# Kernel tuning notes

Measured on AMD Instinct MI355X. Metric: run time of the kernel, lower is better.

## Reference

```python
import jax, jax.numpy as jnp
import numpy as np

FEAT_STRIDE = 16
RPN_NEG, RPN_POS = 0.3, 0.7
FG_FRAC, RPN_BATCH = 0.5, 256
BATCH, NGT, FH, FW = 32, 20, 64, 100
A = 9


def generate_anchors(base_size=16, ratios=(0.5, 1.0, 2.0), scales=(8, 16, 32)):
    base = np.array([0, 0, base_size - 1, base_size - 1], dtype=np.float64)
    w = base[2] - base[0] + 1
    h = base[3] - base[1] + 1
    cx = base[0] + 0.5 * (w - 1)
    cy = base[1] + 0.5 * (h - 1)
    size = w * h
    anchors = []
    for r in ratios:
        ws = np.round(np.sqrt(size / r))
        hs = np.round(ws * r)
        for s in scales:
            W, H = ws * s, hs * s
            anchors.append([cx - 0.5 * (W - 1), cy - 0.5 * (H - 1),
                            cx + 0.5 * (W - 1), cy + 0.5 * (H - 1)])
    return np.array(anchors, dtype=np.float32)


def bbox_overlaps_batch(anchors, gt_boxes):
    # anchors (T,4), gt_boxes (B,K,5) -> (B,T,K)
    gt = gt_boxes[:, :, :4]
    gw = gt[:, :, 2] - gt[:, :, 0] + 1.0
    gh = gt[:, :, 3] - gt[:, :, 1] + 1.0
    gt_area = (gw * gh)[:, None, :]                      # (B,1,K)
    aw = anchors[:, 2] - anchors[:, 0] + 1.0
    ah = anchors[:, 3] - anchors[:, 1] + 1.0
    a_area = (aw * ah)[None, :, None]                    # (1,T,1)
    gt_zero = ((gw == 1.0) & (gh == 1.0))[:, None, :]
    a_zero = ((aw == 1.0) & (ah == 1.0))[None, :, None]
    iw = jnp.minimum(anchors[None, :, None, 2], gt[:, None, :, 2]) - \
         jnp.maximum(anchors[None, :, None, 0], gt[:, None, :, 0]) + 1.0
    ih = jnp.minimum(anchors[None, :, None, 3], gt[:, None, :, 3]) - \
         jnp.maximum(anchors[None, :, None, 1], gt[:, None, :, 1]) + 1.0
    inter = jnp.maximum(iw, 0.0) * jnp.maximum(ih, 0.0)
    ua = a_area + gt_area - inter
    ov = inter / ua
    ov = jnp.where(gt_zero, 0.0, ov)
    ov = jnp.where(a_zero, -1.0, ov)
    return ov


def bbox_transform_batch(ex_rois, gt_rois):
    # ex_rois (T,4), gt_rois (B,T,4) -> (B,T,4)
    ew = ex_rois[:, 2] - ex_rois[:, 0] + 1.0
    eh = ex_rois[:, 3] - ex_rois[:, 1] + 1.0
    ecx = ex_rois[:, 0] + 0.5 * ew
    ecy = ex_rois[:, 1] + 0.5 * eh
    gw = gt_rois[:, :, 2] - gt_rois[:, :, 0] + 1.0
    gh = gt_rois[:, :, 3] - gt_rois[:, :, 1] + 1.0
    gcx = gt_rois[:, :, 0] + 0.5 * gw
    gcy = gt_rois[:, :, 1] + 0.5 * gh
    dx = (gcx - ecx[None, :]) / ew[None, :]
    dy = (gcy - ecy[None, :]) / eh[None, :]
    dw = jnp.log(gw / ew[None, :])
    dh = jnp.log(gh / eh[None, :])
    return jnp.stack([dx, dy, dw, dh], axis=2)


def _rank_per_row(pri):
    # rank of each element within its row after ascending sort
    return jnp.argsort(jnp.argsort(pri, axis=1), axis=1)


def setup_inputs() -> dict:
    key = jax.random.key(0)
    k1, k2, k3 = jax.random.split(key, 3)
    rpn_cls_score = jax.random.normal(k1, (BATCH, 2 * A, FH, FW), dtype=jnp.float32)
    img_h, img_w = float(FH * FEAT_STRIDE), float(FW * FEAT_STRIDE)
    x1 = jax.random.uniform(k2, (BATCH, NGT)) * (img_w * 0.6)
    y1 = jax.random.uniform(k3, (BATCH, NGT)) * (img_h * 0.6)
    bw = 16.0 + jax.random.uniform(jax.random.fold_in(key, 1), (BATCH, NGT)) * 300.0
    bh = 16.0 + jax.random.uniform(jax.random.fold_in(key, 2), (BATCH, NGT)) * 300.0
    x2 = jnp.minimum(x1 + bw, img_w - 1.0)
    y2 = jnp.minimum(y1 + bh, img_h - 1.0)
    cls = jnp.ones((BATCH, NGT))
    gt = jnp.stack([x1, y1, x2, y2, cls], axis=2)
    valid = (jnp.arange(NGT) < 15).astype(jnp.float32)  # last 5 rows: zero padding
    gt = (gt * valid[None, :, None]).astype(jnp.float32)
    im_info = jnp.tile(jnp.array([[img_h, img_w, 1.0]], dtype=jnp.float32), (BATCH, 1))
    num_boxes = jnp.full((BATCH,), 15, dtype=jnp.int32)
    return {"rpn_cls_score": rpn_cls_score, "gt_boxes": gt,
            "im_info": im_info, "num_boxes": num_boxes}


def reference(rpn_cls_score, gt_boxes, im_info, num_boxes):
    B = gt_boxes.shape[0]
    H, W = rpn_cls_score.shape[2], rpn_cls_score.shape[3]
    anchors0 = jnp.asarray(generate_anchors())           # (A,4)
    sx = jnp.arange(W, dtype=jnp.float32) * FEAT_STRIDE
    sy = jnp.arange(H, dtype=jnp.float32) * FEAT_STRIDE
    SX, SY = jnp.meshgrid(sx, sy)                        # 'xy' indexing, (H,W)
    shifts = jnp.stack([SX.ravel(), SY.ravel(), SX.ravel(), SY.ravel()], axis=1)
    all_anchors = (anchors0[None, :, :] + shifts[:, None, :]).reshape(-1, 4)  # (T,4)
    T = all_anchors.shape[0]

    img_h, img_w = im_info[0, 0], im_info[0, 1]
    inside = (all_anchors[:, 0] >= 0) & (all_anchors[:, 1] >= 0) & \
             (all_anchors[:, 2] < img_w) & (all_anchors[:, 3] < img_h)  # (T,)

    ov = bbox_overlaps_batch(all_anchors, gt_boxes)      # (B,T,K)
    ov_in = jnp.where(inside[None, :, None], ov, -2.0)   # exclude border anchors
    max_ov = jnp.max(ov_in, axis=2)                      # (B,T)
    argmax_ov = jnp.argmax(ov_in, axis=2)                # (B,T)
    gt_max = jnp.max(ov_in, axis=1)                      # (B,K)

    labels = jnp.full((B, T), -1.0, dtype=jnp.float32)
    labels = jnp.where(max_ov < RPN_NEG, 0.0, labels)    # bg (no clobber)
    gt_max = jnp.where(gt_max == 0.0, 1e-5, gt_max)
    keep = jnp.sum((ov_in == gt_max[:, None, :]).astype(jnp.int32), axis=2)
    labels = jnp.where(keep > 0, 1.0, labels)            # best anchor per gt
    labels = jnp.where(max_ov >= RPN_POS, 1.0, labels)   # fg by threshold
    labels = jnp.where(inside[None, :], labels, -1.0)

    # --- random fg/bg subsampling (vectorized random permutation) ---
    key = jax.random.key(42)
    kf, kb = jax.random.split(key)
    num_fg = int(FG_FRAC * RPN_BATCH)
    pri_fg = jnp.where(labels == 1.0, jax.random.uniform(kf, (B, T)), jnp.inf)
    rank_fg = _rank_per_row(pri_fg)
    labels = jnp.where((labels == 1.0) & (rank_fg >= num_fg), -1.0, labels)
    num_bg = RPN_BATCH - jnp.sum((labels == 1.0).astype(jnp.int32), axis=1)  # (B,)
    pri_bg = jnp.where(labels == 0.0, jax.random.uniform(kb, (B, T)), jnp.inf)
    rank_bg = _rank_per_row(pri_bg)
    labels = jnp.where((labels == 0.0) & (rank_bg >= num_bg[:, None]), -1.0, labels)

    gt_assigned = jnp.take_along_axis(gt_boxes, argmax_ov[:, :, None], axis=1)  # (B,T,5)
    bbox_targets = bbox_transform_batch(all_anchors, gt_assigned[:, :, :4])     # (B,T,4)
    bbox_targets = jnp.where(inside[None, :, None], bbox_targets, 0.0)

    bbox_in_w = jnp.where(labels == 1.0, 1.0, 0.0)       # RPN_BBOX_INSIDE_WEIGHTS[0]=1
    num_examples = jnp.sum((labels >= 0.0).astype(jnp.float32), axis=1)         # (B,)
    uw = (1.0 / num_examples)[:, None]
    bbox_out_w = jnp.where((labels == 1.0) | (labels == 0.0), uw, 0.0)

    # --- reshape to dense output layout ---
    labels_o = labels.reshape(B, H, W, A).transpose(0, 3, 1, 2).reshape(B, 1, A * H, W)
    targets_o = bbox_targets.reshape(B, H, W, A * 4).transpose(0, 3, 1, 2)
    in_w_o = jnp.broadcast_to(bbox_in_w[:, :, None], (B, T, 4)) \
        .reshape(B, H, W, 4 * A).transpose(0, 3, 1, 2)
    out_w_o = jnp.broadcast_to(bbox_out_w[:, :, None], (B, T, 4)) \
        .reshape(B, H, W, 4 * A).transpose(0, 3, 1, 2)
    return labels_o, targets_o, in_w_o, out_w_o
```

## Files before the change

### kernel.cpp

```cpp
#include <hip/hip_runtime.h>
#include <stdint.h>

#define JAX_PARTITIONABLE 1

static constexpr int B_   = 32;
static constexpr int NGT_ = 20;
static constexpr int H_   = 64;
static constexpr int W_   = 100;
static constexpr int A_   = 9;
static constexpr int HW_  = H_ * W_;
static constexpr int T_   = HW_ * A_;
static constexpr int NBLK_ = T_ / 256;
static constexpr uint32_t NUMFG_ = 128u;
static constexpr uint32_t RPNBATCH_ = 256u;
static constexpr int OUT0_ = B_ * T_;
static constexpr int OUTC_ = B_ * 4 * A_ * HW_;

struct TF2 { uint32_t a, b; };

__host__ __device__ constexpr uint32_t rotl32(uint32_t v, int r) {
  return (v << r) | (v >> (32 - r));
}

__host__ __device__ constexpr TF2 tf2x32(uint32_t k0, uint32_t k1,
                                         uint32_t x0, uint32_t x1) {
  uint32_t ks2 = k0 ^ k1 ^ 0x1BD11BDAu;
  x0 += k0; x1 += k1;
#define TFR_(r) x0 += x1; x1 = rotl32(x1, (r)); x1 ^= x0;
  TFR_(13) TFR_(15) TFR_(26) TFR_(6)
  x0 += k1;  x1 += ks2 + 1u;
  TFR_(17) TFR_(29) TFR_(16) TFR_(24)
  x0 += ks2; x1 += k0 + 2u;
  TFR_(13) TFR_(15) TFR_(26) TFR_(6)
  x0 += k0;  x1 += k1 + 3u;
  TFR_(17) TFR_(29) TFR_(16) TFR_(24)
  x0 += k1;  x1 += ks2 + 4u;
  TFR_(13) TFR_(15) TFR_(26) TFR_(6)
  x0 += ks2; x1 += k0 + 5u;
#undef TFR_
  return TF2{x0, x1};
}

#if JAX_PARTITIONABLE
static constexpr TF2 KFk = tf2x32(0u, 42u, 0u, 0u);
static constexpr TF2 KBk = tf2x32(0u, 42u, 0u, 1u);
static constexpr uint32_t KF0 = KFk.a, KF1 = KFk.b;
static constexpr uint32_t KB0 = KBk.a, KB1 = KBk.b;
#else
static constexpr TF2 R02 = tf2x32(0u, 42u, 0u, 2u);
static constexpr TF2 R13 = tf2x32(0u, 42u, 1u, 3u);
static constexpr uint32_t KF0 = R02.a, KF1 = R13.a;
static constexpr uint32_t KB0 = R02.b, KB1 = R13.b;
#endif

__device__ inline uint32_t mant23(uint32_t k0, uint32_t k1, uint32_t j) {
#if JAX_PARTITIONABLE
  TF2 r = tf2x32(k0, k1, 0u, j);
  return (r.a ^ r.b) >> 9;
#else
  constexpr uint32_t HALF_ = (uint32_t)((uint64_t)B_ * T_ / 2);
  uint32_t lo = (j < HALF_) ? j : j - HALF_;
  TF2 r = tf2x32(k0, k1, lo, lo + HALF_);
  return ((j < HALF_) ? r.a : r.b) >> 9;
#endif
}

__device__ inline uint32_t fkey(float f) {
  uint32_t u = __float_as_uint(f);
  return (u & 0x80000000u) ? ~u : (u | 0x80000000u);
}

__constant__ float c_anc[9][4] = {
  { -84.f,  -40.f,  99.f,  55.f},
  {-176.f,  -88.f, 191.f, 103.f},
  {-360.f, -184.f, 375.f, 199.f},
  { -56.f,  -56.f,  71.f,  71.f},
  {-120.f, -120.f, 135.f, 135.f},
  {-248.f, -248.f, 263.f, 263.f},
  { -36.f,  -80.f,  51.f,  95.f},
  { -80.f, -168.f,  95.f, 183.f},
  {-168.f, -344.f, 183.f, 359.f},
};

__global__ __launch_bounds__(192) void k1_iou(const float* __restrict__ gt,
                                              const float* __restrict__ im,
                                              uint32_t* __restrict__ gmax,
                                              uint32_t* __restrict__ bkey,
                                              uint32_t* __restrict__ barg) {
#pragma clang fp contract(off)
  const int b = blockIdx.y;
  const int tid = threadIdx.x;
  const int iq = blockIdx.x * 192 + tid;
  __shared__ float4 sbox[NGT_];
  __shared__ float sgar[NGT_];
  __shared__ uint32_t skey[NGT_];
  __shared__ uint32_t smask;

  bool valid = false;
  if (tid < NGT_) {
    const float x1 = gt[(b * NGT_ + tid) * 5 + 0];
    const float y1 = gt[(b * NGT_ + tid) * 5 + 1];
    const float x2 = gt[(b * NGT_ + tid) * 5 + 2];
    const float y2 = gt[(b * NGT_ + tid) * 5 + 3];
    const float gw = x2 - x1 + 1.0f, gh = y2 - y1 + 1.0f;
    valid = !(gw == 1.0f && gh == 1.0f);
    sbox[tid] = make_float4(x1, y1, x2, y2);
    sgar[tid] = gw * gh;
    skey[tid] = 0u;
  }
  unsigned long long mv = __ballot(valid);
  if (tid == 0) smask = (uint32_t)mv;
  __syncthreads();

  const int aa = iq / 1600;
  const int cell0 = (iq % 1600) * 4;
  const float imh = im[0], imw = im[1];
  const float bx1 = c_anc[aa][0], by1 = c_anc[aa][1];
  const float bx2 = c_anc[aa][2], by2 = c_anc[aa][3];

  float ax1[4], ay1[4], ax2[4], ay2[4], aarea[4];
  bool ins[4];
#pragma unroll
  for (int c = 0; c < 4; ++c) {
    const int cell = cell0 + c;
    const int wx = cell % W_, hy = cell / W_;
    ax1[c] = bx1 + wx * 16.0f;
    ay1[c] = by1 + hy * 16.0f;
    ax2[c] = bx2 + wx * 16.0f;
    ay2[c] = by2 + hy * 16.0f;
    ins[c] = (ax1[c] >= 0.0f) && (ay1[c] >= 0.0f) && (ax2[c] < imw) && (ay2[c] < imh);
    aarea[c] = (ax2[c] - ax1[c] + 1.0f) * (ay2[c] - ay1[c] + 1.0f);
  }

  uint32_t bk[4] = {0u, 0u, 0u, 0u};
  uint32_t ba[4] = {0u, 0u, 0u, 0u};
  const uint32_t mask = smask;
  const bool anyin = __ballot(ins[0] || ins[1] || ins[2] || ins[3]) != 0ull;

  if (anyin) {
    for (int g = 0; g < NGT_; ++g) {
      if (!((mask >> g) & 1u)) continue;
      const float4 gb = sbox[g];
      const float gar = sgar[g];
      uint32_t gm = 0u;
#pragma unroll
      for (int c = 0; c < 4; ++c) {
        float iw = fminf(ax2[c], gb.z) - fmaxf(ax1[c], gb.x) + 1.0f;
        float ih = fminf(ay2[c], gb.w) - fmaxf(ay1[c], gb.y) + 1.0f;
        float inter = fmaxf(iw, 0.0f) * fmaxf(ih, 0.0f);
        float ua = aarea[c] + gar - inter;
        float ov = inter / ua;
        uint32_t k = ins[c] ? fkey(ov) : 0u;
        if (k > bk[c]) { bk[c] = k; ba[c] = (uint32_t)g; }
        gm = k > gm ? k : gm;
      }
      for (int d = 1; d < 64; d <<= 1) {
        uint32_t o = (uint32_t)__shfl_xor((int)gm, d, 64);
        gm = (o > gm) ? o : gm;
      }
      if ((tid & 63) == 0) atomicMax(&skey[g], gm);
    }
  }
  __syncthreads();
  if (tid < NGT_) atomicMax(&gmax[b * 32 + tid], skey[tid]);

  const size_t base = (size_t)b * T_ + (size_t)aa * HW_ + cell0;
  *(uint4*)(bkey + base) = make_uint4(bk[0], bk[1], bk[2], bk[3]);
  barg[base >> 2] = ba[0] | (ba[1] << 8) | (ba[2] << 16) | (ba[3] << 24);
}

__global__ __launch_bounds__(256) void k2_label(const float* __restrict__ gt,
                                                const float* __restrict__ im,
                                                const uint32_t* __restrict__ gmax,
                                                const uint32_t* __restrict__ bkey,
                                                int8_t* __restrict__ labels,
                                                uint32_t* __restrict__ cntblk,
                                                uint32_t* __restrict__ cand) {
#pragma clang fp contract(off)
  const int b = blockIdx.y;
  const int bx = blockIdx.x;
  const int tid = threadIdx.x;
  const int i = bx * 256 + tid;
  __shared__ float4 sbox[NGT_];
  __shared__ float sgar[NGT_];
  __shared__ uint32_t skey[NGT_];
  __shared__ uint32_t smask, sminG;
  __shared__ uint32_t sfgc[4], sbgc[4];

  bool valid = false;
  uint32_t myk = 0xFFFFFFFFu;
  if (tid < NGT_) {
    const float x1 = gt[(b * NGT_ + tid) * 5 + 0];
    const float y1 = gt[(b * NGT_ + tid) * 5 + 1];
    const float x2 = gt[(b * NGT_ + tid) * 5 + 2];
    const float y2 = gt[(b * NGT_ + tid) * 5 + 3];
    const float gw = x2 - x1 + 1.0f, gh = y2 - y1 + 1.0f;
    valid = !(gw == 1.0f && gh == 1.0f);
    sbox[tid] = make_float4(x1, y1, x2, y2);
    sgar[tid] = gw * gh;
    const uint32_t gk = gmax[b * 32 + tid];
    skey[tid] = gk;
    if (valid && gk > 0x80000000u) myk = gk;
  }
  unsigned long long mv = __ballot(valid);
  uint32_t mn = myk;
  for (int d = 1; d < 64; d <<= 1) {
    uint32_t o = (uint32_t)__shfl_xor((int)mn, d, 64);
    mn = (o < mn) ? o : mn;
  }
  if (tid == 0) { smask = (uint32_t)mv; sminG = mn; }
  __syncthreads();

  const int a = i / HW_, cell = i % HW_;
  const int t = cell * A_ + a;
  const float imh = im[0], imw = im[1];
  const float ax1 = c_anc[a][0] + (cell % W_) * 16.0f;
  const float ay1 = c_anc[a][1] + (cell / W_) * 16.0f;
  const float ax2 = c_anc[a][2] + (cell % W_) * 16.0f;
  const float ay2 = c_anc[a][3] + (cell / W_) * 16.0f;
  const bool inside = (ax1 >= 0.0f) && (ay1 >= 0.0f) && (ax2 < imw) && (ay2 < imh);
  const float aarea = (ax2 - ax1 + 1.0f) * (ay2 - ay1 + 1.0f);

  const uint32_t bk = bkey[(size_t)b * T_ + i];
  const float maxovf = __uint_as_float(bk & 0x7FFFFFFFu);

  int lab = -1;
  if (inside && maxovf < 0.3f) lab = 0;

  bool haskeep = false;
  const bool needck = inside && bk >= sminG && maxovf < 0.7f;
  if (__ballot(needck) != 0ull) {
    const uint32_t mask = smask;
    for (int g = 0; g < NGT_; ++g) {
      if (!((mask >> g) & 1u)) continue;
      const float4 gb = sbox[g];
      const float gar = sgar[g];
      float iw = fminf(ax2, gb.z) - fmaxf(ax1, gb.x) + 1.0f;
      float ih = fminf(ay2, gb.w) - fmaxf(ay1, gb.y) + 1.0f;
      float inter = fmaxf(iw, 0.0f) * fmaxf(ih, 0.0f);
      float ua = aarea + gar - inter;
      float ov = inter / ua;
      const uint32_t gk = skey[g];
      if (needck && gk > 0x80000000u && fkey(ov) == gk) haskeep = true;
    }
  }
  if (haskeep) lab = 1;
  if (inside && maxovf >= 0.7f) lab = 1;
  labels[(size_t)b * T_ + i] = (int8_t)lab;

  uint32_t m = 0;
  if (lab >= 0)
    m = mant23(lab ? KF0 : KB0, lab ? KF1 : KB1, (uint32_t)(b * T_ + t));

  const int wv = tid >> 6, lane = tid & 63;
  const unsigned long long mk1 = __ballot(lab == 1);
  const unsigned long long mk0 = __ballot(lab == 0);
  if (lane == 0) { sfgc[wv] = (uint32_t)__popcll(mk1); sbgc[wv] = (uint32_t)__popcll(mk0); }
  __syncthreads();
  uint32_t fgbase = 0, bgbase = 0, fgtot = 0, bgtot = 0;
  for (int w2 = 0; w2 < 4; ++w2) {
    if (w2 < wv) { fgbase += sfgc[w2]; bgbase += sbgc[w2]; }
    fgtot += sfgc[w2]; bgtot += sbgc[w2];
  }
  const unsigned long long lmask = (1ull << lane) - 1ull;
  if (lab == 1) {
    uint32_t off = fgbase + (uint32_t)__popcll(mk1 & lmask);
    cand[((size_t)0 * B_ + b) * T_ + (size_t)bx * 256 + off] = m;
  } else if (lab == 0) {
    uint32_t off = bgbase + (uint32_t)__popcll(mk0 & lmask);
    cand[((size_t)1 * B_ + b) * T_ + (size_t)bx * 256 + off] = m;
  }
  if (tid == 0) {
    cntblk[(0 * B_ + b) * NBLK_ + bx] = fgtot;
    cntblk[(1 * B_ + b) * NBLK_ + bx] = bgtot;
  }
}

__device__ inline void find_kth1024(uint32_t* hist, int n, uint32_t target, int tid,
                                    uint32_t* wsum, uint32_t* res) {
  const int C = n >> 10;
  const int base = tid * C;
  uint32_t s = 0;
  for (int i = 0; i < C; ++i) s += hist[base + i];
  uint32_t v = s;
  for (int d = 1; d < 64; d <<= 1) {
    uint32_t u = (uint32_t)__shfl_up((int)v, d, 64);
    if ((tid & 63) >= d) v += u;
  }
  const int wv = tid >> 6;
  if ((tid & 63) == 63) wsum[wv] = v;
  __syncthreads();
  uint32_t woff = 0;
  for (int w2 = 0; w2 < wv; ++w2) woff += wsum[w2];
  uint32_t c = woff + v - s;
  for (int i = 0; i < C; ++i) {
    uint32_t h = hist[base + i];
    if (h != 0u && target >= c && target < c + h) {
      res[0] = (uint32_t)(base + i);
      res[1] = c;
    }
    c += h;
  }
  __syncthreads();
}

__global__ __launch_bounds__(1024) void k3_select(const int8_t* __restrict__ labels,
                                                  const uint32_t* __restrict__ cntblk,
                                                  const uint32_t* __restrict__ cand,
                                                  uint32_t* __restrict__ cnt,
                                                  uint32_t* __restrict__ sel) {
  const int b = blockIdx.x >> 1;
  const int cls = blockIdx.x & 1;
  const int tid = threadIdx.x;
  __shared__ uint32_t scnt[NBLK_];
  __shared__ uint32_t hist[4096];
  __shared__ uint32_t wsum[16];
  __shared__ uint32_t res[2];
  __shared__ uint32_t lcnt, sTot, sCf;

  if (tid == 0) { sTot = 0u; sCf = 0u; }
  __syncthreads();
  if (tid < NBLK_) {
    uint32_t c = cntblk[(cls * B_ + b) * NBLK_ + tid];
    scnt[tid] = c;
    atomicAdd(&sTot, c);
    if (cls == 1) atomicAdd(&sCf, cntblk[(0 * B_ + b) * NBLK_ + tid]);
  }
  __syncthreads();
  const uint32_t n = sTot;
  const uint32_t cf = (cls == 0) ? n : sCf;
  if (tid == 0) cnt[b * 2 + cls] = n;
  const uint32_t fgk = cf < NUMFG_ ? cf : NUMFG_;
  const uint32_t K = (cls == 0) ? NUMFG_ : RPNBATCH_ - fgk;
  if (n <= K) {
    if (tid == 0) { sel[b * 4 + cls * 2] = 0xFFFFFFFFu; sel[b * 4 + cls * 2 + 1] = 0xFFFFFFFFu; }
    return;
  }
  const uint32_t* list = cand + ((size_t)cls * B_ + b) * T_;

  for (int i = tid; i < 2048; i += 1024) hist[i] = 0u;
  __syncthreads();
  for (int gi = tid; gi < T_; gi += 1024)
    if ((uint32_t)(gi & 255) < scnt[gi >> 8]) atomicAdd(&hist[list[gi] >> 12], 1u);
  __syncthreads();
  find_kth1024(hist, 2048, K - 1u, tid, wsum, res);
  const uint32_t b1 = res[0], cb1 = res[1];
  __syncthreads();

  for (int i = tid; i < 4096; i += 1024) hist[i] = 0u;
  __syncthreads();
  for (int gi = tid; gi < T_; gi += 1024)
    if ((uint32_t)(gi & 255) < scnt[gi >> 8]) {
      uint32_t m = list[gi];
      if ((m >> 12) == b1) atomicAdd(&hist[m & 0xFFFu], 1u);
    }
  __syncthreads();
  find_kth1024(hist, 4096, K - 1u - cb1, tid, wsum, res);
  const uint32_t b2 = res[0], cb2 = res[1];
  const uint32_t Mstar = (b1 << 12) | b2;
  const uint32_t need = K - cb1 - cb2;
  const uint32_t cnteq = hist[b2];
  __syncthreads();

  uint32_t tstar = 0xFFFFFFFFu;
  if (need < cnteq) {
    const int8_t want = (cls == 0) ? (int8_t)1 : (int8_t)0;
    const uint32_t k0 = (cls == 0) ? KF0 : KB0;
    const uint32_t k1 = (cls == 0) ? KF1 : KB1;
    const int8_t* lrow = labels + (size_t)b * T_;
    if (tid == 0) lcnt = 0u;
    __syncthreads();
    for (int s = tid; s < T_; s += 1024) {
      if (lrow[s] == want) {
        int aa = s / HW_, cc = s % HW_;
        uint32_t t = (uint32_t)(cc * A_ + aa);
        if (mant23(k0, k1, (uint32_t)b * (uint32_t)T_ + t) == Mstar) {
          uint32_t p = atomicAdd(&lcnt, 1u);
          if (p < 4096u) hist[p] = t;
        }
      }
    }
    __syncthreads();
    if (tid == 0) {
      uint32_t nn = lcnt < 4096u ? lcnt : 4096u;
      uint32_t prev = 0u;
      for (uint32_t kk = 0; kk < need; ++kk) {
        uint32_t mn2 = 0xFFFFFFFFu;
        for (uint32_t i2 = 0; i2 < nn; ++i2) {
          uint32_t vv = hist[i2];
          if ((kk == 0u || vv > prev) && vv < mn2) mn2 = vv;
        }
        prev = mn2;
      }
      tstar = prev;
    }
  }
  if (tid == 0) { sel[b * 4 + cls * 2] = Mstar; sel[b * 4 + cls * 2 + 1] = tstar; }
}

__global__ __launch_bounds__(256) void k4_final(const float* __restrict__ gt,
                                                const float* __restrict__ im,
                                                const int8_t* __restrict__ labels,
                                                const int8_t* __restrict__ argmax8,
                                                const uint32_t* __restrict__ cnt,
                                                const uint32_t* __restrict__ sel,
                                                float* __restrict__ out) {
#pragma clang fp contract(off)
  const int b = blockIdx.y;
  const int tid = threadIdx.x;
  const int i = blockIdx.x * 256 + tid;
  __shared__ float sgt[NGT_ * 5];
  if (tid < NGT_ * 5) sgt[tid] = gt[b * NGT_ * 5 + tid];
  __syncthreads();

  const int a = i / HW_, cell = i % HW_;
  const int t = cell * A_ + a;
  const float imh = im[0], imw = im[1];
  const float ax1 = c_anc[a][0] + (cell % W_) * 16.0f;
  const float ay1 = c_anc[a][1] + (cell / W_) * 16.0f;
  const float ax2 = c_anc[a][2] + (cell % W_) * 16.0f;
  const float ay2 = c_anc[a][3] + (cell / W_) * 16.0f;
  const bool inside = (ax1 >= 0.0f) && (ay1 >= 0.0f) && (ax2 < imw) && (ay2 < imh);

  int lab = labels[(size_t)b * T_ + i];
  const uint32_t j = (uint32_t)(b * T_ + t);
  if (lab == 1) {
    uint32_t m = mant23(KF0, KF1, j);
    uint32_t Ms = sel[b * 4 + 0], ts = sel[b * 4 + 1];
    if (!(m < Ms || (m == Ms && (uint32_t)t <= ts))) lab = -1;
  } else if (lab == 0) {
    uint32_t m = mant23(KB0, KB1, j);
    uint32_t Ms = sel[b * 4 + 2], ts = sel[b * 4 + 3];
    if (!(m < Ms || (m == Ms && (uint32_t)t <= ts))) lab = -1;
  }

  const uint32_t cf = cnt[b * 2 + 0];
  const uint32_t cbn = cnt[b * 2 + 1];
  const uint32_t fgk = cf < NUMFG_ ? cf : NUMFG_;
  const uint32_t nbg = RPNBATCH_ - fgk;
  const uint32_t bgk = cbn < nbg ? cbn : nbg;
  const float uw = 1.0f / (float)(fgk + bgk);

  float tg0 = 0.f, tg1 = 0.f, tg2 = 0.f, tg3 = 0.f;
  if (inside) {
    const int bg_ = argmax8[(size_t)b * T_ + i];
    const float gx1 = sgt[bg_ * 5], gy1 = sgt[bg_ * 5 + 1];
    const float gx2 = sgt[bg_ * 5 + 2], gy2 = sgt[bg_ * 5 + 3];
    const float ew = ax2 - ax1 + 1.0f, eh = ay2 - ay1 + 1.0f;
    const float ecx = ax1 + 0.5f * ew, ecy = ay1 + 0.5f * eh;
    const float gw = gx2 - gx1 + 1.0f, gh = gy2 - gy1 + 1.0f;
    const float gcx = gx1 + 0.5f * gw, gcy = gy1 + 0.5f * gh;
    tg0 = (gcx - ecx) / ew;
    tg1 = (gcy - ecy) / eh;
    tg2 = logf(gw / ew);
    tg3 = logf(gh / eh);
  }
  const float inw = (lab == 1) ? 1.0f : 0.0f;
  const float oww = (lab == 1 || lab == 0) ? uw : 0.0f;

  out[(size_t)b * T_ + i] = (float)lab;
  const size_t ch = ((size_t)b * 36 + (size_t)a * 4) * HW_ + cell;
  float* o1 = out + OUT0_;
  o1[ch] = tg0; o1[ch + HW_] = tg1; o1[ch + 2 * HW_] = tg2; o1[ch + 3 * HW_] = tg3;
  float* o2 = o1 + OUTC_;
  o2[ch] = inw; o2[ch + HW_] = inw; o2[ch + 2 * HW_] = inw; o2[ch + 3 * HW_] = inw;
  float* o3 = o2 + OUTC_;
  o3[ch] = oww; o3[ch + HW_] = oww; o3[ch + 2 * HW_] = oww; o3[ch + 3 * HW_] = oww;
}

extern "C" void kernel_launch(void* const* d_in, const int* in_sizes, int n_in,
                              void* d_out, int out_size, void* d_ws, size_t ws_size,
                              hipStream_t stream) {
  (void)in_sizes; (void)n_in; (void)out_size; (void)ws_size;
  const float* gt = (const float*)d_in[1];
  const float* im = (const float*)d_in[2];
  float* out = (float*)d_out;

  uint8_t* ws = (uint8_t*)d_ws;
  uint32_t* gmax   = (uint32_t*)(ws + 0);
  uint32_t* cnt    = (uint32_t*)(ws + 4096);
  uint32_t* sel    = (uint32_t*)(ws + 4352);
  uint32_t* cntblk = (uint32_t*)(ws + 4864);
  int8_t*   labels = (int8_t*)  (ws + 62464);
  uint32_t* barg   = (uint32_t*)(ws + 1905664);
  uint32_t* bkey   = (uint32_t*)(ws + 3748864);
  uint32_t* cand   = (uint32_t*)(ws + 11121664);

  (void)hipMemsetAsync(ws, 0, 4096, stream);

  k1_iou<<<dim3(75, B_), dim3(192), 0, stream>>>(gt, im, gmax, bkey, barg);
  k2_label<<<dim3(NBLK_, B_), dim3(256), 0, stream>>>(gt, im, gmax, bkey, labels, cntblk, cand);
  k3_select<<<dim3(B_ * 2), dim3(1024), 0, stream>>>(labels, cntblk, cand, cnt, sel);
  k4_final<<<dim3(NBLK_, B_), dim3(256), 0, stream>>>(gt, im, labels, (const int8_t*)barg,
                                                      cnt, sel, out);
}
```

Before: 208.8 us.

## Fuse selection into label kernel via last-block pattern and vectorize per-thread work

Removes the memset and the separate select kernel: k1 writes per-block gt max partials instead of atomics, k2 reduces them itself, and the last block per batch (tracked by an atomic counter) runs the histogram top-k selection. k2 and k4 now process four anchors per thread with vector loads and float4 stores. The cost is that the selection runs on a single 192-thread block per batch rather than 1024-thread blocks, and it adds extra shared memory to every k2 block.

Result: slower. 537.6 us (+157.5%).

```diff
diff --git a/kernel.cpp b/kernel.cpp
--- a/kernel.cpp
+++ b/kernel.cpp
@@ -1,5 +1,6 @@
 #include <hip/hip_runtime.h>
 #include <stdint.h>
+#include <stddef.h>
 
 #define JAX_PARTITIONABLE 1
 
@@ -10,7 +11,8 @@
 static constexpr int A_   = 9;
 static constexpr int HW_  = H_ * W_;
 static constexpr int T_   = HW_ * A_;
-static constexpr int NBLK_ = T_ / 256;
+static constexpr int NB2_ = 75;
+static constexpr int SEG_ = 768;
 static constexpr uint32_t NUMFG_ = 128u;
 static constexpr uint32_t RPNBATCH_ = 256u;
 static constexpr int OUT0_ = B_ * T_;
@@ -84,17 +86,21 @@
 
 __global__ __launch_bounds__(192) void k1_iou(const float* __restrict__ gt,
                                               const float* __restrict__ im,
-                                              uint32_t* __restrict__ gmax,
+                                              uint32_t* __restrict__ gpart,
                                               uint32_t* __restrict__ bkey,
-                                              uint32_t* __restrict__ barg) {
+                                              uint32_t* __restrict__ barg,
+                                              uint32_t* __restrict__ dcnt) {
 #pragma clang fp contract(off)
   const int b = blockIdx.y;
+  const int bx = blockIdx.x;
   const int tid = threadIdx.x;
-  const int iq = blockIdx.x * 192 + tid;
+  const int iq = bx * 192 + tid;
   __shared__ float4 sbox[NGT_];
   __shared__ float sgar[NGT_];
   __shared__ uint32_t skey[NGT_];
   __shared__ uint32_t smask;
+
+  if (bx == 0 && tid == 0) dcnt[b] = 0u;
 
   bool valid = false;
   if (tid < NGT_) {
@@ -162,33 +168,71 @@
     }
   }
   __syncthreads();
-  if (tid < NGT_) atomicMax(&gmax[b * 32 + tid], skey[tid]);
+  if (tid < NGT_) gpart[(b * NGT_ + tid) * NB2_ + bx] = skey[tid];
 
   const size_t base = (size_t)b * T_ + (size_t)aa * HW_ + cell0;
   *(uint4*)(bkey + base) = make_uint4(bk[0], bk[1], bk[2], bk[3]);
   barg[base >> 2] = ba[0] | (ba[1] << 8) | (ba[2] << 16) | (ba[3] << 24);
 }
 
-__global__ __launch_bounds__(256) void k2_label(const float* __restrict__ gt,
+__device__ inline void find_kth128(uint32_t* hist, int n, uint32_t target, int tid,
+                                   uint32_t* wsum, uint32_t* res) {
+  const int C = n >> 7;
+  uint32_t s = 0, v = 0;
+  int base = 0;
+  if (tid < 128) {
+    base = tid * C;
+    for (int i = 0; i < C; ++i) s += hist[base + i];
+    v = s;
+    for (int d = 1; d < 64; d <<= 1) {
+      uint32_t u = (uint32_t)__shfl_up((int)v, d, 64);
+      if ((tid & 63) >= d) v += u;
+    }
+    if ((tid & 63) == 63) wsum[tid >> 6] = v;
+  }
+  __syncthreads();
+  if (tid < 128) {
+    uint32_t woff = (tid >= 64) ? wsum[0] : 0u;
+    uint32_t c = woff + v - s;
+    for (int i = 0; i < C; ++i) {
+      uint32_t h = hist[base + i];
+      if (h != 0u && target >= c && target < c + h) {
+        res[0] = (uint32_t)(base + i);
+        res[1] = c;
+      }
+      c += h;
+    }
+  }
+  __syncthreads();
+}
+
+__global__ __launch_bounds__(192) void k2_label(const float* __restrict__ gt,
                                                 const float* __restrict__ im,
-                                                const uint32_t* __restrict__ gmax,
+                                                const uint32_t* __restrict__ gpart,
                                                 const uint32_t* __restrict__ bkey,
                                                 int8_t* __restrict__ labels,
                                                 uint32_t* __restrict__ cntblk,
-                                                uint32_t* __restrict__ cand) {
+                                                uint32_t* __restrict__ cand,
+                                                uint32_t* __restrict__ dcnt,
+                                                uint32_t* __restrict__ cnt,
+                                                uint32_t* __restrict__ sel) {
 #pragma clang fp contract(off)
   const int b = blockIdx.y;
   const int bx = blockIdx.x;
   const int tid = threadIdx.x;
-  const int i = bx * 256 + tid;
+  const int iq = bx * 192 + tid;
   __shared__ float4 sbox[NGT_];
   __shared__ float sgar[NGT_];
   __shared__ uint32_t skey[NGT_];
-  __shared__ uint32_t smask, sminG;
-  __shared__ uint32_t sfgc[4], sbgc[4];
+  __shared__ uint32_t smask, sminG, sflag;
+  __shared__ uint32_t swc[3];
+  __shared__ uint32_t scnt2[2][NB2_];
+  __shared__ uint32_t hist[4096];
+  __shared__ uint32_t wsum[2];
+  __shared__ uint32_t res[2];
+  __shared__ uint32_t lcnt, stot[2];
 
   bool valid = false;
-  uint32_t myk = 0xFFFFFFFFu;
   if (tid < NGT_) {
     const float x1 = gt[(b * NGT_ + tid) * 5 + 0];
     const float y1 = gt[(b * NGT_ + tid) * 5 + 1];
@@ -198,274 +242,301 @@
     valid = !(gw == 1.0f && gh == 1.0f);
     sbox[tid] = make_float4(x1, y1, x2, y2);
     sgar[tid] = gw * gh;
-    const uint32_t gk = gmax[b * 32 + tid];
-    skey[tid] = gk;
-    if (valid && gk > 0x80000000u) myk = gk;
+    skey[tid] = 0u;
   }
   unsigned long long mv = __ballot(valid);
-  uint32_t mn = myk;
-  for (int d = 1; d < 64; d <<= 1) {
-    uint32_t o = (uint32_t)__shfl_xor((int)mn, d, 64);
-    mn = (o < mn) ? o : mn;
-  }
-  if (tid == 0) { smask = (uint32_t)mv; sminG = mn; }
-  __syncthreads();
-
-  const int a = i / HW_, cell = i % HW_;
-  const int t = cell * A_ + a;
+  if (tid == 0) smask = (uint32_t)mv;
+  __syncthreads();
+  for (int idx = tid; idx < NGT_ * NB2_; idx += 192)
+    atomicMax(&skey[idx / NB2_], gpart[b * NGT_ * NB2_ + idx]);
+  __syncthreads();
+  if (tid < 64) {
+    uint32_t kk = 0xFFFFFFFFu;
+    if (tid < NGT_ && ((smask >> tid) & 1u)) {
+      uint32_t g = skey[tid];
+      if (g > 0x80000000u) kk = g;
+    }
+    for (int d = 1; d < 64; d <<= 1) {
+      uint32_t o = (uint32_t)__shfl_xor((int)kk, d, 64);
+      kk = (o < kk) ? o : kk;
+    }
+    if (tid == 0) sminG = kk;
+  }
+  __syncthreads();
+
+  const int aa = iq / 1600;
+  const int cell0 = (iq % 1600) * 4;
   const float imh = im[0], imw = im[1];
-  const float ax1 = c_anc[a][0] + (cell % W_) * 16.0f;
-  const float ay1 = c_anc[a][1] + (cell / W_) * 16.0f;
-  const float ax2 = c_anc[a][2] + (cell % W_) * 16.0f;
-  const float ay2 = c_anc[a][3] + (cell / W_) * 16.0f;
-  const bool inside = (ax1 >= 0.0f) && (ay1 >= 0.0f) && (ax2 < imw) && (ay2 < imh);
-  const float aarea = (ax2 - ax1 + 1.0f) * (ay2 - ay1 + 1.0f);
-
-  const uint32_t bk = bkey[(size_t)b * T_ + i];
-  const float maxovf = __uint_as_float(bk & 0x7FFFFFFFu);
-
-  int lab = -1;
-  if (inside && maxovf < 0.3f) lab = 0;
-
-  bool haskeep = false;
-  const bool needck = inside && bk >= sminG && maxovf < 0.7f;
-  if (__ballot(needck) != 0ull) {
+  const float bx1 = c_anc[aa][0], by1 = c_anc[aa][1];
+  const float bx2 = c_anc[aa][2], by2 = c_anc[aa][3];
+  const size_t base = (size_t)b * T_ + (size_t)aa * HW_ + cell0;
+  const uint4 bk4 = *(const uint4*)(bkey + base);
+
+  float ax1[4], ay1[4], ax2[4], ay2[4], aarea[4];
+  bool ins[4], need[4];
+  uint32_t bkv[4] = {bk4.x, bk4.y, bk4.z, bk4.w};
+  int lab[4];
+#pragma unroll
+  for (int c = 0; c < 4; ++c) {
+    const int cell = cell0 + c;
+    const int wx = cell % W_, hy = cell / W_;
+    ax1[c] = bx1 + wx * 16.0f;
+    ay1[c] = by1 + hy * 16.0f;
+    ax2[c] = bx2 + wx * 16.0f;
+    ay2[c] = by2 + hy * 16.0f;
+    ins[c] = (ax1[c] >= 0.0f) && (ay1[c] >= 0.0f) && (ax2[c] < imw) && (ay2[c] < imh);
+    aarea[c] = (ax2[c] - ax1[c] + 1.0f) * (ay2[c] - ay1[c] + 1.0f);
+    const float mo = __uint_as_float(bkv[c] & 0x7FFFFFFFu);
+    lab[c] = -1;
+    if (ins[c] && mo < 0.3f) lab[c] = 0;
+    need[c] = ins[c] && bkv[c] >= sminG && mo < 0.7f;
+    if (ins[c] && mo >= 0.7f) lab[c] = 1;
+  }
+  if (__ballot(need[0] || need[1] || need[2] || need[3]) != 0ull) {
     const uint32_t mask = smask;
     for (int g = 0; g < NGT_; ++g) {
       if (!((mask >> g) & 1u)) continue;
+      const uint32_t gk = skey[g];
+      if (gk <= 0x80000000u) continue;
       const float4 gb = sbox[g];
       const float gar = sgar[g];
-      float iw = fminf(ax2, gb.z) - fmaxf(ax1, gb.x) + 1.0f;
-      float ih = fminf(ay2, gb.w) - fmaxf(ay1, gb.y) + 1.0f;
-      float inter = fmaxf(iw, 0.0f) * fmaxf(ih, 0.0f);
-      float ua = aarea + gar - inter;
-      float ov = inter / ua;
-      const uint32_t gk = skey[g];
-      if (needck && gk > 0x80000000u && fkey(ov) == gk) haskeep = true;
-    }
-  }
-  if (haskeep) lab = 1;
-  if (inside && maxovf >= 0.7f) lab = 1;
-  labels[(size_t)b * T_ + i] = (int8_t)lab;
-
-  uint32_t m = 0;
-  if (lab >= 0)
-    m = mant23(lab ? KF0 : KB0, lab ? KF1 : KB1, (uint32_t)(b * T_ + t));
-
-  const int wv = tid >> 6, lane = tid & 63;
-  const unsigned long long mk1 = __ballot(lab == 1);
-  const unsigned long long mk0 = __ballot(lab == 0);
-  if (lane == 0) { sfgc[wv] = (uint32_t)__popcll(mk1); sbgc[wv] = (uint32_t)__popcll(mk0); }
-  __syncthreads();
-  uint32_t fgbase = 0, bgbase = 0, fgtot = 0, bgtot = 0;
-  for (int w2 = 0; w2 < 4; ++w2) {
-    if (w2 < wv) { fgbase += sfgc[w2]; bgbase += sbgc[w2]; }
-    fgtot += sfgc[w2]; bgtot += sbgc[w2];
-  }
-  const unsigned long long lmask = (1ull << lane) - 1ull;
-  if (lab == 1) {
-    uint32_t off = fgbase + (uint32_t)__popcll(mk1 & lmask);
-    cand[((size_t)0 * B_ + b) * T_ + (size_t)bx * 256 + off] = m;
-  } else if (lab == 0) {
-    uint32_t off = bgbase + (uint32_t)__popcll(mk0 & lmask);
-    cand[((size_t)1 * B_ + b) * T_ + (size_t)bx * 256 + off] = m;
+#pragma unroll
+      for (int c = 0; c < 4; ++c) {
+        if (!need[c]) continue;
+        float iw = fminf(ax2[c], gb.z) - fmaxf(ax1[c], gb.x) + 1.0f;
+        float ih = fminf(ay2[c], gb.w) - fmaxf(ay1[c], gb.y) + 1.0f;
+        float inter = fmaxf(iw, 0.0f) * fmaxf(ih, 0.0f);
+        float ua = aarea[c] + gar - inter;
+        float ov = inter / ua;
+        if (fkey(ov) == gk) lab[c] = 1;
+      }
+    }
+  }
+
+  uint32_t lpack = 0, mant[4];
+  int nf = 0, nb = 0;
+#pragma unroll
+  for (int c = 0; c < 4; ++c) {
+    lpack |= ((uint32_t)(uint8_t)(int8_t)lab[c]) << (8 * c);
+    mant[c] = 0u;
+    if (lab[c] >= 0) {
+      const int t = (cell0 + c) * A_ + aa;
+      mant[c] = mant23(lab[c] ? KF0 : KB0, lab[c] ? KF1 : KB1, (uint32_t)(b * T_ + t));
+      if (lab[c] == 1) ++nf; else ++nb;
+    }
+  }
+  *(uint32_t*)(labels + base) = lpack;
+
+  const int lane = tid & 63, wv = tid >> 6;
+  uint32_t cpk = (uint32_t)nf | ((uint32_t)nb << 16);
+  uint32_t incl = cpk;
+  for (int d = 1; d < 64; d <<= 1) {
+    uint32_t u = (uint32_t)__shfl_up((int)incl, d, 64);
+    if (lane >= d) incl += u;
+  }
+  uint32_t wtot = (uint32_t)__shfl((int)incl, 63, 64);
+  if (lane == 0) swc[wv] = wtot;
+  __syncthreads();
+  uint32_t woffF = 0, woffB = 0, totF = 0, totB = 0;
+  for (int w = 0; w < 3; ++w) {
+    uint32_t v = swc[w];
+    if (w < wv) { woffF += v & 0xFFFFu; woffB += v >> 16; }
+    totF += v & 0xFFFFu; totB += v >> 16;
+  }
+  uint32_t excl = incl - cpk;
+  uint32_t posF = woffF + (excl & 0xFFFFu);
+  uint32_t posB = woffB + (excl >> 16);
+  uint32_t* dstF = cand + ((size_t)0 * B_ + b) * T_ + (size_t)bx * SEG_;
+  uint32_t* dstB = cand + ((size_t)1 * B_ + b) * T_ + (size_t)bx * SEG_;
+#pragma unroll
+  for (int c = 0; c < 4; ++c) {
+    if (lab[c] == 1) dstF[posF++] = mant[c];
+    else if (lab[c] == 0) dstB[posB++] = mant[c];
   }
   if (tid == 0) {
-    cntblk[(0 * B_ + b) * NBLK_ + bx] = fgtot;
-    cntblk[(1 * B_ + b) * NBLK_ + bx] = bgtot;
-  }
-}
-
-__device__ inline void find_kth1024(uint32_t* hist, int n, uint32_t target, int tid,
-                                    uint32_t* wsum, uint32_t* res) {
-  const int C = n >> 10;
-  const int base = tid * C;
-  uint32_t s = 0;
-  for (int i = 0; i < C; ++i) s += hist[base + i];
-  uint32_t v = s;
-  for (int d = 1; d < 64; d <<= 1) {
-    uint32_t u = (uint32_t)__shfl_up((int)v, d, 64);
-    if ((tid & 63) >= d) v += u;
-  }
-  const int wv = tid >> 6;
-  if ((tid & 63) == 63) wsum[wv] = v;
-  __syncthreads();
-  uint32_t woff = 0;
-  for (int w2 = 0; w2 < wv; ++w2) woff += wsum[w2];
-  uint32_t c = woff + v - s;
-  for (int i = 0; i < C; ++i) {
-    uint32_t h = hist[base + i];
-    if (h != 0u && target >= c && target < c + h) {
-      res[0] = (uint32_t)(base + i);
-      res[1] = c;
-    }
-    c += h;
-  }
-  __syncthreads();
-}
-
-__global__ __launch_bounds__(1024) void k3_select(const int8_t* __restrict__ labels,
-                                                  const uint32_t* __restrict__ cntblk,
-                                                  const uint32_t* __restrict__ cand,
-                                                  uint32_t* __restrict__ cnt,
-                                                  uint32_t* __restrict__ sel) {
-  const int b = blockIdx.x >> 1;
-  const int cls = blockIdx.x & 1;
-  const int tid = threadIdx.x;
-  __shared__ uint32_t scnt[NBLK_];
-  __shared__ uint32_t hist[4096];
-  __shared__ uint32_t wsum[16];
-  __shared__ uint32_t res[2];
-  __shared__ uint32_t lcnt, sTot, sCf;
-
-  if (tid == 0) { sTot = 0u; sCf = 0u; }
-  __syncthreads();
-  if (tid < NBLK_) {
-    uint32_t c = cntblk[(cls * B_ + b) * NBLK_ + tid];
-    scnt[tid] = c;
-    atomicAdd(&sTot, c);
-    if (cls == 1) atomicAdd(&sCf, cntblk[(0 * B_ + b) * NBLK_ + tid]);
-  }
-  __syncthreads();
-  const uint32_t n = sTot;
-  const uint32_t cf = (cls == 0) ? n : sCf;
-  if (tid == 0) cnt[b * 2 + cls] = n;
-  const uint32_t fgk = cf < NUMFG_ ? cf : NUMFG_;
-  const uint32_t K = (cls == 0) ? NUMFG_ : RPNBATCH_ - fgk;
-  if (n <= K) {
-    if (tid == 0) { sel[b * 4 + cls * 2] = 0xFFFFFFFFu; sel[b * 4 + cls * 2 + 1] = 0xFFFFFFFFu; }
-    return;
-  }
-  const uint32_t* list = cand + ((size_t)cls * B_ + b) * T_;
-
-  for (int i = tid; i < 2048; i += 1024) hist[i] = 0u;
-  __syncthreads();
-  for (int gi = tid; gi < T_; gi += 1024)
-    if ((uint32_t)(gi & 255) < scnt[gi >> 8]) atomicAdd(&hist[list[gi] >> 12], 1u);
-  __syncthreads();
-  find_kth1024(hist, 2048, K - 1u, tid, wsum, res);
-  const uint32_t b1 = res[0], cb1 = res[1];
-  __syncthreads();
-
-  for (int i = tid; i < 4096; i += 1024) hist[i] = 0u;
-  __syncthreads();
-  for (int gi = tid; gi < T_; gi += 1024)
-    if ((uint32_t)(gi & 255) < scnt[gi >> 8]) {
-      uint32_t m = list[gi];
-      if ((m >> 12) == b1) atomicAdd(&hist[m & 0xFFFu], 1u);
-    }
-  __syncthreads();
-  find_kth1024(hist, 4096, K - 1u - cb1, tid, wsum, res);
-  const uint32_t b2 = res[0], cb2 = res[1];
-  const uint32_t Mstar = (b1 << 12) | b2;
-  const uint32_t need = K - cb1 - cb2;
-  const uint32_t cnteq = hist[b2];
-  __syncthreads();
-
-  uint32_t tstar = 0xFFFFFFFFu;
-  if (need < cnteq) {
-    const int8_t want = (cls == 0) ? (int8_t)1 : (int8_t)0;
-    const uint32_t k0 = (cls == 0) ? KF0 : KB0;
-    const uint32_t k1 = (cls == 0) ? KF1 : KB1;
-    const int8_t* lrow = labels + (size_t)b * T_;
-    if (tid == 0) lcnt = 0u;
+    cntblk[(0 * B_ + b) * NB2_ + bx] = totF;
+    cntblk[(1 * B_ + b) * NB2_ + bx] = totB;
+  }
+
+  __threadfence();
+  __syncthreads();
+  if (tid == 0) sflag = (atomicAdd(&dcnt[b], 1u) == (uint32_t)(NB2_ - 1)) ? 1u : 0u;
+  __syncthreads();
+  if (!sflag) return;
+  __threadfence();
+
+  if (tid == 0) { stot[0] = 0u; stot[1] = 0u; }
+  __syncthreads();
+  for (int idx = tid; idx < 2 * NB2_; idx += 192) {
+    const int cls = idx / NB2_, sx = idx % NB2_;
+    const uint32_t v = cntblk[(cls * B_ + b) * NB2_ + sx];
+    scnt2[cls][sx] = v;
+    atomicAdd(&stot[cls], v);
+  }
+  __syncthreads();
+  const uint32_t cf = stot[0], cbn = stot[1];
+  if (tid == 0) { cnt[b * 2 + 0] = cf; cnt[b * 2 + 1] = cbn; }
+
+  for (int cls = 0; cls < 2; ++cls) {
+    const uint32_t fgk = cf < NUMFG_ ? cf : NUMFG_;
+    const uint32_t K = (cls == 0) ? NUMFG_ : RPNBATCH_ - fgk;
+    const uint32_t n = (cls == 0) ? cf : cbn;
+    if (n <= K) {
+      if (tid == 0) { sel[b * 4 + cls * 2] = 0xFFFFFFFFu; sel[b * 4 + cls * 2 + 1] = 0xFFFFFFFFu; }
+      __syncthreads();
+      continue;
+    }
+    const uint32_t* list = cand + ((size_t)cls * B_ + b) * T_;
+
+    for (int i2 = tid; i2 < 2048; i2 += 192) hist[i2] = 0u;
     __syncthreads();
-    for (int s = tid; s < T_; s += 1024) {
-      if (lrow[s] == want) {
-        int aa = s / HW_, cc = s % HW_;
-        uint32_t t = (uint32_t)(cc * A_ + aa);
-        if (mant23(k0, k1, (uint32_t)b * (uint32_t)T_ + t) == Mstar) {
-          uint32_t p = atomicAdd(&lcnt, 1u);
-          if (p < 4096u) hist[p] = t;
+    for (int gi = tid; gi < T_; gi += 192) {
+      const int seg = gi / SEG_, off = gi - seg * SEG_;
+      if ((uint32_t)off < scnt2[cls][seg]) atomicAdd(&hist[list[gi] >> 12], 1u);
+    }
+    __syncthreads();
+    find_kth128(hist, 2048, K - 1u, tid, wsum, res);
+    const uint32_t b1 = res[0], cb1 = res[1];
+
+    for (int i2 = tid; i2 < 4096; i2 += 192) hist[i2] = 0u;
+    __syncthreads();
+    for (int gi = tid; gi < T_; gi += 192) {
+      const int seg = gi / SEG_, off = gi - seg * SEG_;
+      if ((uint32_t)off < scnt2[cls][seg]) {
+        const uint32_t m = list[gi];
+        if ((m >> 12) == b1) atomicAdd(&hist[m & 0xFFFu], 1u);
+      }
+    }
+    __syncthreads();
+    find_kth128(hist, 4096, K - 1u - cb1, tid, wsum, res);
+    const uint32_t b2 = res[0], cb2 = res[1];
+    const uint32_t Mstar = (b1 << 12) | b2;
+    const uint32_t need2 = K - cb1 - cb2;
+    const uint32_t cnteq = hist[b2];
+    __syncthreads();
+
+    uint32_t tstar = 0xFFFFFFFFu;
+    if (need2 < cnteq) {
+      const int8_t want = (cls == 0) ? (int8_t)1 : (int8_t)0;
+      const uint32_t k0 = (cls == 0) ? KF0 : KB0;
+      const uint32_t k1 = (cls == 0) ? KF1 : KB1;
+      const int8_t* lrow = labels + (size_t)b * T_;
+      if (tid == 0) lcnt = 0u;
+      __syncthreads();
+      for (int s = tid; s < T_; s += 192) {
+        if (lrow[s] == want) {
+          const int aa2 = s / HW_, cc = s % HW_;
+          const uint32_t t = (uint32_t)(cc * A_ + aa2);
+          if (mant23(k0, k1, (uint32_t)b * (uint32_t)T_ + t) == Mstar) {
+            const uint32_t p = atomicAdd(&lcnt, 1u);
+            if (p < 4096u) hist[p] = t;
+          }
         }
       }
-    }
+      __syncthreads();
+      if (tid == 0) {
+        const uint32_t nn = lcnt < 4096u ? lcnt : 4096u;
+        uint32_t prev = 0u;
+        for (uint32_t kk2 = 0; kk2 < need2; ++kk2) {
+          uint32_t mn2 = 0xFFFFFFFFu;
+          for (uint32_t i3 = 0; i3 < nn; ++i3) {
+            const uint32_t vv = hist[i3];
+            if ((kk2 == 0u || vv > prev) && vv < mn2) mn2 = vv;
+          }
+          prev = mn2;
+        }
+        tstar = prev;
+      }
+    }
+    if (tid == 0) { sel[b * 4 + cls * 2] = Mstar; sel[b * 4 + cls * 2 + 1] = tstar; }
     __syncthreads();
-    if (tid == 0) {
-      uint32_t nn = lcnt < 4096u ? lcnt : 4096u;
-      uint32_t prev = 0u;
-      for (uint32_t kk = 0; kk < need; ++kk) {
-        uint32_t mn2 = 0xFFFFFFFFu;
-        for (uint32_t i2 = 0; i2 < nn; ++i2) {
-          uint32_t vv = hist[i2];
-          if ((kk == 0u || vv > prev) && vv < mn2) mn2 = vv;
-        }
-        prev = mn2;
-      }
-      tstar = prev;
-    }
-  }
-  if (tid == 0) { sel[b * 4 + cls * 2] = Mstar; sel[b * 4 + cls * 2 + 1] = tstar; }
-}
-
-__global__ __launch_bounds__(256) void k4_final(const float* __restrict__ gt,
+  }
+}
+
+__global__ __launch_bounds__(192) void k4_final(const float* __restrict__ gt,
                                                 const float* __restrict__ im,
                                                 const int8_t* __restrict__ labels,
-                                                const int8_t* __restrict__ argmax8,
+                                                const uint32_t* __restrict__ barg,
                                                 const uint32_t* __restrict__ cnt,
                                                 const uint32_t* __restrict__ sel,
                                                 float* __restrict__ out) {
 #pragma clang fp contract(off)
   const int b = blockIdx.y;
   const int tid = threadIdx.x;
-  const int i = blockIdx.x * 256 + tid;
+  const int iq = blockIdx.x * 192 + tid;
   __shared__ float sgt[NGT_ * 5];
   if (tid < NGT_ * 5) sgt[tid] = gt[b * NGT_ * 5 + tid];
   __syncthreads();
 
-  const int a = i / HW_, cell = i % HW_;
-  const int t = cell * A_ + a;
+  const int aa = iq / 1600;
+  const int cell0 = (iq % 1600) * 4;
   const float imh = im[0], imw = im[1];
-  const float ax1 = c_anc[a][0] + (cell % W_) * 16.0f;
-  const float ay1 = c_anc[a][1] + (cell / W_) * 16.0f;
-  const float ax2 = c_anc[a][2] + (cell % W_) * 16.0f;
-  const float ay2 = c_anc[a][3] + (cell / W_) * 16.0f;
-  const bool inside = (ax1 >= 0.0f) && (ay1 >= 0.0f) && (ax2 < imw) && (ay2 < imh);
-
-  int lab = labels[(size_t)b * T_ + i];
-  const uint32_t j = (uint32_t)(b * T_ + t);
-  if (lab == 1) {
-    uint32_t m = mant23(KF0, KF1, j);
-    uint32_t Ms = sel[b * 4 + 0], ts = sel[b * 4 + 1];
-    if (!(m < Ms || (m == Ms && (uint32_t)t <= ts))) lab = -1;
-  } else if (lab == 0) {
-    uint32_t m = mant23(KB0, KB1, j);
-    uint32_t Ms = sel[b * 4 + 2], ts = sel[b * 4 + 3];
-    if (!(m < Ms || (m == Ms && (uint32_t)t <= ts))) lab = -1;
-  }
-
-  const uint32_t cf = cnt[b * 2 + 0];
-  const uint32_t cbn = cnt[b * 2 + 1];
+  const size_t base = (size_t)b * T_ + (size_t)aa * HW_ + cell0;
+  const uint32_t lv = *(const uint32_t*)(labels + base);
+  const uint32_t av = barg[base >> 2];
+  const uint32_t Ms1 = sel[b * 4 + 0], ts1 = sel[b * 4 + 1];
+  const uint32_t Ms0 = sel[b * 4 + 2], ts0 = sel[b * 4 + 3];
+  const uint32_t cf = cnt[b * 2 + 0], cbn = cnt[b * 2 + 1];
   const uint32_t fgk = cf < NUMFG_ ? cf : NUMFG_;
   const uint32_t nbg = RPNBATCH_ - fgk;
   const uint32_t bgk = cbn < nbg ? cbn : nbg;
   const float uw = 1.0f / (float)(fgk + bgk);
-
-  float tg0 = 0.f, tg1 = 0.f, tg2 = 0.f, tg3 = 0.f;
-  if (inside) {
-    const int bg_ = argmax8[(size_t)b * T_ + i];
-    const float gx1 = sgt[bg_ * 5], gy1 = sgt[bg_ * 5 + 1];
-    const float gx2 = sgt[bg_ * 5 + 2], gy2 = sgt[bg_ * 5 + 3];
-    const float ew = ax2 - ax1 + 1.0f, eh = ay2 - ay1 + 1.0f;
-    const float ecx = ax1 + 0.5f * ew, ecy = ay1 + 0.5f * eh;
-    const float gw = gx2 - gx1 + 1.0f, gh = gy2 - gy1 + 1.0f;
-    const float gcx = gx1 + 0.5f * gw, gcy = gy1 + 0.5f * gh;
-    tg0 = (gcx - ecx) / ew;
-    tg1 = (gcy - ecy) / eh;
-    tg2 = logf(gw / ew);
-    tg3 = logf(gh / eh);
-  }
-  const float inw = (lab == 1) ? 1.0f : 0.0f;
-  const float oww = (lab == 1 || lab == 0) ? uw : 0.0f;
-
-  out[(size_t)b * T_ + i] = (float)lab;
-  const size_t ch = ((size_t)b * 36 + (size_t)a * 4) * HW_ + cell;
+  const float bx1 = c_anc[aa][0], by1 = c_anc[aa][1];
+  const float bx2 = c_anc[aa][2], by2 = c_anc[aa][3];
+
+  float labf[4], inwf[4], owwf[4], tg[4][4];
+#pragma unroll
+  for (int c = 0; c < 4; ++c) {
+    const int cell = cell0 + c;
+    const int wx = cell % W_, hy = cell / W_;
+    const float ax1 = bx1 + wx * 16.0f, ay1 = by1 + hy * 16.0f;
+    const float ax2 = bx2 + wx * 16.0f, ay2 = by2 + hy * 16.0f;
+    const bool inside = (ax1 >= 0.0f) && (ay1 >= 0.0f) && (ax2 < imw) && (ay2 < imh);
+    int lab = (int)(int8_t)(uint8_t)(lv >> (8 * c));
+    const uint32_t t = (uint32_t)(cell * A_ + aa);
+    const uint32_t j = (uint32_t)(b * T_) + t;
+    if (lab == 1) {
+      const uint32_t m = mant23(KF0, KF1, j);
+      if (!(m < Ms1 || (m == Ms1 && t <= ts1))) lab = -1;
+    } else if (lab == 0) {
+      const uint32_t m = mant23(KB0, KB1, j);
+      if (!(m < Ms0 || (m == Ms0 && t <= ts0))) lab = -1;
+    }
+    float t0 = 0.f, t1 = 0.f, t2 = 0.f, t3 = 0.f;
+    if (inside) {
+      const int bg = (int)((av >> (8 * c)) & 0xFFu);
+      const float gx1 = sgt[bg * 5], gy1 = sgt[bg * 5 + 1];
+      const float gx2 = sgt[bg * 5 + 2], gy2 = sgt[bg * 5 + 3];
+      const float ew = ax2 - ax1 + 1.0f, eh = ay2 - ay1 + 1.0f;
+      const float ecx = ax1 + 0.5f * ew, ecy = ay1 + 0.5f * eh;
+      const float gw = gx2 - gx1 + 1.0f, gh = gy2 - gy1 + 1.0f;
+      const float gcx = gx1 + 0.5f * gw, gcy = gy1 + 0.5f * gh;
+      t0 = (gcx - ecx) / ew;
+      t1 = (gcy - ecy) / eh;
+      t2 = logf(gw / ew);
+      t3 = logf(gh / eh);
+    }
+    tg[0][c] = t0; tg[1][c] = t1; tg[2][c] = t2; tg[3][c] = t3;
+    labf[c] = (float)lab;
+    inwf[c] = (lab == 1) ? 1.0f : 0.0f;
+    owwf[c] = (lab == 1 || lab == 0) ? uw : 0.0f;
+  }
+
+  *(float4*)(out + base) = make_float4(labf[0], labf[1], labf[2], labf[3]);
+  const size_t ch = ((size_t)b * 36 + (size_t)aa * 4) * HW_ + cell0;
   float* o1 = out + OUT0_;
-  o1[ch] = tg0; o1[ch + HW_] = tg1; o1[ch + 2 * HW_] = tg2; o1[ch + 3 * HW_] = tg3;
   float* o2 = o1 + OUTC_;
-  o2[ch] = inw; o2[ch + HW_] = inw; o2[ch + 2 * HW_] = inw; o2[ch + 3 * HW_] = inw;
   float* o3 = o2 + OUTC_;
-  o3[ch] = oww; o3[ch + HW_] = oww; o3[ch + 2 * HW_] = oww; o3[ch + 3 * HW_] = oww;
+#pragma unroll
+  for (int k = 0; k < 4; ++k)
+    *(float4*)(o1 + ch + (size_t)k * HW_) = make_float4(tg[k][0], tg[k][1], tg[k][2], tg[k][3]);
+  const float4 iv = make_float4(inwf[0], inwf[1], inwf[2], inwf[3]);
+  const float4 ovv = make_float4(owwf[0], owwf[1], owwf[2], owwf[3]);
+#pragma unroll
+  for (int k = 0; k < 4; ++k) {
+    *(float4*)(o2 + ch + (size_t)k * HW_) = iv;
+    *(float4*)(o3 + ch + (size_t)k * HW_) = ovv;
+  }
 }
 
 extern "C" void kernel_launch(void* const* d_in, const int* in_sizes, int n_in,
@@ -477,20 +548,18 @@
   float* out = (float*)d_out;
 
   uint8_t* ws = (uint8_t*)d_ws;
-  uint32_t* gmax   = (uint32_t*)(ws + 0);
-  uint32_t* cnt    = (uint32_t*)(ws + 4096);
-  uint32_t* sel    = (uint32_t*)(ws + 4352);
-  uint32_t* cntblk = (uint32_t*)(ws + 4864);
-  int8_t*   labels = (int8_t*)  (ws + 62464);
-  uint32_t* barg   = (uint32_t*)(ws + 1905664);
-  uint32_t* bkey   = (uint32_t*)(ws + 3748864);
-  uint32_t* cand   = (uint32_t*)(ws + 11121664);
-
-  (void)hipMemsetAsync(ws, 0, 4096, stream);
-
-  k1_iou<<<dim3(75, B_), dim3(192), 0, stream>>>(gt, im, gmax, bkey, barg);
-  k2_label<<<dim3(NBLK_, B_), dim3(256), 0, stream>>>(gt, im, gmax, bkey, labels, cntblk, cand);
-  k3_select<<<dim3(B_ * 2), dim3(1024), 0, stream>>>(labels, cntblk, cand, cnt, sel);
-  k4_final<<<dim3(NBLK_, B_), dim3(256), 0, stream>>>(gt, im, labels, (const int8_t*)barg,
-                                                      cnt, sel, out);
-}
+  uint32_t* gpart  = (uint32_t*)(ws + 0);
+  uint32_t* cnt    = (uint32_t*)(ws + 192000);
+  uint32_t* sel    = (uint32_t*)(ws + 192256);
+  uint32_t* dcnt   = (uint32_t*)(ws + 192768);
+  uint32_t* cntblk = (uint32_t*)(ws + 192896);
+  int8_t*   labels = (int8_t*)  (ws + 212096);
+  uint32_t* barg   = (uint32_t*)(ws + 2055296);
+  uint32_t* bkey   = (uint32_t*)(ws + 3898496);
+  uint32_t* cand   = (uint32_t*)(ws + 11271296);
+
+  k1_iou<<<dim3(NB2_, B_), dim3(192), 0, stream>>>(gt, im, gpart, bkey, barg, dcnt);
+  k2_label<<<dim3(NB2_, B_), dim3(192), 0, stream>>>(gt, im, gpart, bkey, labels,
+                                                     cntblk, cand, dcnt, cnt, sel);
+  k4_final<<<dim3(NB2_, B_), dim3(192), 0, stream>>>(gt, im, labels, barg, cnt, sel, out);
+}
```
